# Optimization experiments

Measured on AMD Instinct MI355X. Metric: run time of the kernel, lower is better.

The kernel has to match this reference:

```python
import jax, jax.numpy as jnp
import numpy as np


def setup_inputs() -> dict:
    key = jax.random.key(0)
    ks = jax.random.split(key, 6)
    B, R, H, E, D = 64, 2048, 1024, 512, 1024
    hidden_states = jax.random.normal(ks[0], (B, H), dtype=jnp.float32)
    att_feats = jax.random.normal(ks[1], (B, R, D), dtype=jnp.float32)
    p_att_feats = jax.random.normal(ks[2], (B, R, E), dtype=jnp.float32)
    att_masks = jnp.zeros((B, R), dtype=jnp.float32)  # additive mask; zeros = unmasked
    w_h = jax.random.normal(ks[3], (H, E), dtype=jnp.float32) * (1.0 / np.sqrt(H))
    w_alpha = jax.random.normal(ks[4], (E,), dtype=jnp.float32) * (1.0 / np.sqrt(E))
    return {"hidden_states": hidden_states, "att_feats": att_feats,
            "p_att_feats": p_att_feats, "att_masks": att_masks,
            "w_h": w_h, "w_alpha": w_alpha}


def reference(hidden_states, att_feats, p_att_feats, att_masks, w_h, w_alpha):
    # w_h(hidden_states): [B, E], broadcast over regions R
    wh = hidden_states @ w_h                      # [B, E]
    alpha = jnp.tanh(wh[:, None, :] + p_att_feats)  # [B, R, E]
    # w_alpha reduces E -> scalar per region
    alpha = jnp.einsum('bre,e->br', alpha, w_alpha)  # [B, R]
    alpha = alpha + att_masks                     # additive mask
    alpha = jax.nn.softmax(alpha, axis=-1)        # [B, R]
    # weighted sum over regions: bmm(alpha[:,None,:], att_feats).squeeze(1)
    att = jnp.einsum('br,brd->bd', alpha, att_feats)  # [B, D]
    return att
```

## Files before the change

kernel.cpp:

```cpp
#include <hip/hip_runtime.h>
#include <math.h>

#define BB 64
#define RR 2048
#define HH 1024
#define EE 512
#define DD 1024
#define RC 32
#define RPB (RR / RC)
#define RPW (RPB / 4)

typedef float f32x4 __attribute__((ext_vector_type(4)));

__device__ __forceinline__ float fast_tanh(float x) {
    float e = __expf(2.0f * x);
    return 1.0f - 2.0f * __builtin_amdgcn_rcpf(e + 1.0f);
}

__global__ __launch_bounds__(256) void k_wh(const float* __restrict__ hidden,
                                            const float* __restrict__ w_h,
                                            float* __restrict__ wh) {
    __shared__ float sh[HH];
    __shared__ float sred[4][64];
    const int b = blockIdx.x;
    const int t = threadIdx.x;
    const int lane = t & 63, hseg = t >> 6;
    const int e = blockIdx.y * 64 + lane;
    for (int h = t; h < HH; h += 256) sh[h] = hidden[b * HH + h];
    __syncthreads();
    const int h0 = hseg * 256;
    float acc = 0.f;
#pragma unroll 8
    for (int h = 0; h < 256; ++h) acc = fmaf(sh[h0 + h], w_h[(h0 + h) * EE + e], acc);
    sred[hseg][lane] = acc;
    __syncthreads();
    if (t < 64)
        wh[b * EE + blockIdx.y * 64 + t] =
            (sred[0][t] + sred[1][t]) + (sred[2][t] + sred[3][t]);
}

__global__ __launch_bounds__(256) void k_fused(const float* __restrict__ p_att,
                                               const float* __restrict__ feats,
                                               const float* __restrict__ wh,
                                               const float* __restrict__ w_alpha,
                                               const float* __restrict__ mask,
                                               float* __restrict__ num,
                                               float* __restrict__ den) {
    __shared__ float sw[RPB];
    const int b = blockIdx.x, rc = blockIdx.y;
    const int t = threadIdx.x, wave = t >> 6, lane = t & 63;
    const int r0 = rc * RPB;

    const float* __restrict__ whb = wh + b * EE;
    const f32x4 wh0 = *(const f32x4*)(whb + lane * 4);
    const f32x4 wh1 = *(const f32x4*)(whb + 256 + lane * 4);
    const f32x4 wa0 = *(const f32x4*)(w_alpha + lane * 4);
    const f32x4 wa1 = *(const f32x4*)(w_alpha + 256 + lane * 4);
    const long long rowb = (long long)b * RR + r0 + wave * RPW;
    const f32x4* __restrict__ pb = (const f32x4*)(p_att + rowb * EE);
#pragma unroll 4
    for (int rr = 0; rr < RPW; ++rr) {
        f32x4 p0 = __builtin_nontemporal_load(pb + rr * (EE / 4) + lane);
        f32x4 p1 = __builtin_nontemporal_load(pb + rr * (EE / 4) + 64 + lane);
        float s;
        s = fast_tanh(p0.x + wh0.x) * wa0.x;
        s = fmaf(fast_tanh(p0.y + wh0.y), wa0.y, s);
        s = fmaf(fast_tanh(p0.z + wh0.z), wa0.z, s);
        s = fmaf(fast_tanh(p0.w + wh0.w), wa0.w, s);
        s = fmaf(fast_tanh(p1.x + wh1.x), wa1.x, s);
        s = fmaf(fast_tanh(p1.y + wh1.y), wa1.y, s);
        s = fmaf(fast_tanh(p1.z + wh1.z), wa1.z, s);
        s = fmaf(fast_tanh(p1.w + wh1.w), wa1.w, s);
#pragma unroll
        for (int off = 32; off; off >>= 1) s += __shfl_xor(s, off);
        if (lane == 0) sw[wave * RPW + rr] = __expf(s + mask[rowb + rr]);
    }
    __syncthreads();

    const f32x4* __restrict__ fb =
        (const f32x4*)(feats + ((long long)b * RR + r0) * DD) + t;
    f32x4 acc = {0.f, 0.f, 0.f, 0.f};
#pragma unroll 8
    for (int r = 0; r < RPB; ++r) {
        const float a = sw[r];
        f32x4 f = __builtin_nontemporal_load(fb + r * (DD / 4));
        acc.x = fmaf(a, f.x, acc.x);
        acc.y = fmaf(a, f.y, acc.y);
        acc.z = fmaf(a, f.z, acc.z);
        acc.w = fmaf(a, f.w, acc.w);
    }
    ((f32x4*)(num + (long long)(b * RC + rc) * DD))[t] = acc;
    if (t == 0) {
        float d = 0.f;
#pragma unroll
        for (int r = 0; r < RPB; ++r) d += sw[r];
        den[b * RC + rc] = d;
    }
}

__global__ __launch_bounds__(256) void k_out(const float* __restrict__ num,
                                             const float* __restrict__ den,
                                             float* __restrict__ out) {
    const int idx = blockIdx.x * 256 + threadIdx.x;
    const int b = idx >> 10;
    const int d = idx & 1023;
    float ds = 0.f;
#pragma unroll
    for (int rc = 0; rc < RC; ++rc) ds += den[b * RC + rc];
    float ns = 0.f;
#pragma unroll
    for (int rc = 0; rc < RC; ++rc)
        ns += num[((long long)(b * RC + rc) << 10) + d];
    out[idx] = ns / ds;
}

extern "C" void kernel_launch(void* const* d_in, const int* in_sizes, int n_in,
                              void* d_out, int out_size, void* d_ws, size_t ws_size,
                              hipStream_t stream) {
    const float* hidden  = (const float*)d_in[0];
    const float* feats   = (const float*)d_in[1];
    const float* p_att   = (const float*)d_in[2];
    const float* mask    = (const float*)d_in[3];
    const float* w_h     = (const float*)d_in[4];
    const float* w_alpha = (const float*)d_in[5];
    float* out = (float*)d_out;

    char* ws = (char*)d_ws;
    float* wh  = (float*)(ws);
    float* num = (float*)(ws + (size_t)131072);
    float* den = (float*)(ws + (size_t)(131072 + 8388608));

    k_wh<<<dim3(BB, EE / 64), 256, 0, stream>>>(hidden, w_h, wh);
    k_fused<<<dim3(BB, RC), 256, 0, stream>>>(p_att, feats, wh, w_alpha, mask, num, den);
    k_out<<<(BB * DD) / 256, 256, 0, stream>>>(num, den, out);
}
```

Before: 162.1 us.

## Interleave score and feature accumulation per wave, batch k_wh over multiple rows

The fused kernel no longer computes all softmax weights first and then sweeps features after a barrier. Each wave now weights its own rows' feature vectors as soon as each score is ready, keeping full-width partial sums in registers and reducing the four waves through shared memory at the end. This is meant to overlap the p_att and feature streams and remove the mid-kernel barrier stall, at the cost of more registers and a 16KB shared reduction buffer. Other changes: nontemporal loads are dropped, the grid axes are swapped, and k_wh processes four batch rows per block to reuse w_h loads.

```diff
diff --git a/kernel.cpp b/kernel.cpp
--- a/kernel.cpp
+++ b/kernel.cpp
@@ -9,6 +9,7 @@
 #define RC 32
 #define RPB (RR / RC)
 #define RPW (RPB / 4)
+#define MB 4
 
 typedef float f32x4 __attribute__((ext_vector_type(4)));
 
@@ -17,26 +18,42 @@
     return 1.0f - 2.0f * __builtin_amdgcn_rcpf(e + 1.0f);
 }
 
+__device__ __forceinline__ f32x4 fma4(float a, f32x4 f, f32x4 c) {
+    c.x = fmaf(a, f.x, c.x);
+    c.y = fmaf(a, f.y, c.y);
+    c.z = fmaf(a, f.z, c.z);
+    c.w = fmaf(a, f.w, c.w);
+    return c;
+}
+
 __global__ __launch_bounds__(256) void k_wh(const float* __restrict__ hidden,
                                             const float* __restrict__ w_h,
                                             float* __restrict__ wh) {
-    __shared__ float sh[HH];
-    __shared__ float sred[4][64];
-    const int b = blockIdx.x;
+    __shared__ float sh[MB][HH];
+    __shared__ float sred[4][MB][64];
+    const int b0 = blockIdx.x * MB;
     const int t = threadIdx.x;
     const int lane = t & 63, hseg = t >> 6;
     const int e = blockIdx.y * 64 + lane;
-    for (int h = t; h < HH; h += 256) sh[h] = hidden[b * HH + h];
+    for (int idx = t; idx < MB * HH; idx += 256)
+        ((float*)sh)[idx] = hidden[b0 * HH + idx];
     __syncthreads();
     const int h0 = hseg * 256;
-    float acc = 0.f;
-#pragma unroll 8
-    for (int h = 0; h < 256; ++h) acc = fmaf(sh[h0 + h], w_h[(h0 + h) * EE + e], acc);
-    sred[hseg][lane] = acc;
+    float acc[MB] = {0.f, 0.f, 0.f, 0.f};
+#pragma unroll 4
+    for (int h = 0; h < 256; ++h) {
+        const float wv = w_h[(h0 + h) * EE + e];
+#pragma unroll
+        for (int b = 0; b < MB; ++b) acc[b] = fmaf(sh[b][h0 + h], wv, acc[b]);
+    }
+#pragma unroll
+    for (int b = 0; b < MB; ++b) sred[hseg][b][lane] = acc[b];
     __syncthreads();
-    if (t < 64)
-        wh[b * EE + blockIdx.y * 64 + t] =
-            (sred[0][t] + sred[1][t]) + (sred[2][t] + sred[3][t]);
+    if (t < MB * 64) {
+        const int b = t >> 6, l = t & 63;
+        wh[(b0 + b) * EE + blockIdx.y * 64 + l] =
+            (sred[0][b][l] + sred[1][b][l]) + (sred[2][b][l] + sred[3][b][l]);
+    }
 }
 
 __global__ __launch_bounds__(256) void k_fused(const float* __restrict__ p_att,
@@ -46,22 +63,27 @@
                                                const float* __restrict__ mask,
                                                float* __restrict__ num,
                                                float* __restrict__ den) {
-    __shared__ float sw[RPB];
-    const int b = blockIdx.x, rc = blockIdx.y;
+    __shared__ float snum[4][DD];
+    __shared__ float sden[4];
+    const int rc = blockIdx.x, b = blockIdx.y;
     const int t = threadIdx.x, wave = t >> 6, lane = t & 63;
-    const int r0 = rc * RPB;
 
     const float* __restrict__ whb = wh + b * EE;
     const f32x4 wh0 = *(const f32x4*)(whb + lane * 4);
     const f32x4 wh1 = *(const f32x4*)(whb + 256 + lane * 4);
     const f32x4 wa0 = *(const f32x4*)(w_alpha + lane * 4);
     const f32x4 wa1 = *(const f32x4*)(w_alpha + 256 + lane * 4);
-    const long long rowb = (long long)b * RR + r0 + wave * RPW;
-    const f32x4* __restrict__ pb = (const f32x4*)(p_att + rowb * EE);
-#pragma unroll 4
+
+    const long long row0 = (long long)b * RR + rc * RPB + wave * RPW;
+    const f32x4* __restrict__ pb = (const f32x4*)(p_att + row0 * EE);
+    const f32x4* __restrict__ fb = (const f32x4*)(feats + row0 * DD);
+
+    f32x4 acc0 = {0.f, 0.f, 0.f, 0.f}, acc1 = acc0, acc2 = acc0, acc3 = acc0;
+    float dsum = 0.f;
+#pragma unroll 2
     for (int rr = 0; rr < RPW; ++rr) {
-        f32x4 p0 = __builtin_nontemporal_load(pb + rr * (EE / 4) + lane);
-        f32x4 p1 = __builtin_nontemporal_load(pb + rr * (EE / 4) + 64 + lane);
+        f32x4 p0 = pb[rr * (EE / 4) + lane];
+        f32x4 p1 = pb[rr * (EE / 4) + 64 + lane];
         float s;
         s = fast_tanh(p0.x + wh0.x) * wa0.x;
         s = fmaf(fast_tanh(p0.y + wh0.y), wa0.y, s);
@@ -73,29 +95,27 @@
         s = fmaf(fast_tanh(p1.w + wh1.w), wa1.w, s);
 #pragma unroll
         for (int off = 32; off; off >>= 1) s += __shfl_xor(s, off);
-        if (lane == 0) sw[wave * RPW + rr] = __expf(s + mask[rowb + rr]);
+        const float w = __expf(s + mask[row0 + rr]);
+        dsum += w;
+        const f32x4* __restrict__ fr = fb + rr * (DD / 4);
+        acc0 = fma4(w, fr[lane], acc0);
+        acc1 = fma4(w, fr[64 + lane], acc1);
+        acc2 = fma4(w, fr[128 + lane], acc2);
+        acc3 = fma4(w, fr[192 + lane], acc3);
     }
+    *(f32x4*)&snum[wave][0 + lane * 4] = acc0;
+    *(f32x4*)&snum[wave][256 + lane * 4] = acc1;
+    *(f32x4*)&snum[wave][512 + lane * 4] = acc2;
+    *(f32x4*)&snum[wave][768 + lane * 4] = acc3;
+    if (lane == 0) sden[wave] = dsum;
     __syncthreads();
-
-    const f32x4* __restrict__ fb =
-        (const f32x4*)(feats + ((long long)b * RR + r0) * DD) + t;
-    f32x4 acc = {0.f, 0.f, 0.f, 0.f};
-#pragma unroll 8
-    for (int r = 0; r < RPB; ++r) {
-        const float a = sw[r];
-        f32x4 f = __builtin_nontemporal_load(fb + r * (DD / 4));
-        acc.x = fmaf(a, f.x, acc.x);
-        acc.y = fmaf(a, f.y, acc.y);
-        acc.z = fmaf(a, f.z, acc.z);
-        acc.w = fmaf(a, f.w, acc.w);
-    }
-    ((f32x4*)(num + (long long)(b * RC + rc) * DD))[t] = acc;
-    if (t == 0) {
-        float d = 0.f;
-#pragma unroll
-        for (int r = 0; r < RPB; ++r) d += sw[r];
-        den[b * RC + rc] = d;
-    }
+    f32x4 r0 = *(const f32x4*)&snum[0][t * 4];
+    f32x4 r1 = *(const f32x4*)&snum[1][t * 4];
+    f32x4 r2 = *(const f32x4*)&snum[2][t * 4];
+    f32x4 r3 = *(const f32x4*)&snum[3][t * 4];
+    f32x4 r = (r0 + r1) + (r2 + r3);
+    ((f32x4*)(num + (long long)(b * RC + rc) * DD))[t] = r;
+    if (t == 0) den[b * RC + rc] = (sden[0] + sden[1]) + (sden[2] + sden[3]);
 }
 
 __global__ __launch_bounds__(256) void k_out(const float* __restrict__ num,
@@ -130,7 +150,7 @@
     float* num = (float*)(ws + (size_t)131072);
     float* den = (float*)(ws + (size_t)(131072 + 8388608));
 
-    k_wh<<<dim3(BB, EE / 64), 256, 0, stream>>>(hidden, w_h, wh);
-    k_fused<<<dim3(BB, RC), 256, 0, stream>>>(p_att, feats, wh, w_alpha, mask, num, den);
+    k_wh<<<dim3(BB / MB, EE / 64), 256, 0, stream>>>(hidden, w_h, wh);
+    k_fused<<<dim3(RC, BB), 256, 0, stream>>>(p_att, feats, wh, w_alpha, mask, num, den);
     k_out<<<(BB * DD) / 256, 256, 0, stream>>>(num, den, out);
 }
```

New measurement: 199.3 us. 22.9% more time.

## Batch four rows per k_wh block and halve region chunks in fused kernel

Applied to the files above, without the earlier changes.

k_wh now handles four batch rows per block, so each w_h element loaded from global memory feeds four accumulators. This cuts w_h traffic fourfold and launches fewer blocks. Separately, RC drops from 32 to 16, so each k_fused block covers twice as many regions. That halves the partial-sum buffer and the k_out reduction work, but leaves 1024 fused blocks with longer serial loops, which may hide memory latency less well.

```diff
diff --git a/kernel.cpp b/kernel.cpp
--- a/kernel.cpp
+++ b/kernel.cpp
@@ -6,9 +6,10 @@
 #define HH 1024
 #define EE 512
 #define DD 1024
-#define RC 32
+#define RC 16
 #define RPB (RR / RC)
 #define RPW (RPB / 4)
+#define MB 4
 
 typedef float f32x4 __attribute__((ext_vector_type(4)));
 
@@ -20,23 +21,31 @@
 __global__ __launch_bounds__(256) void k_wh(const float* __restrict__ hidden,
                                             const float* __restrict__ w_h,
                                             float* __restrict__ wh) {
-    __shared__ float sh[HH];
-    __shared__ float sred[4][64];
-    const int b = blockIdx.x;
+    __shared__ float sh[MB][HH];
+    __shared__ float sred[4][MB][64];
+    const int b0 = blockIdx.x * MB;
     const int t = threadIdx.x;
     const int lane = t & 63, hseg = t >> 6;
     const int e = blockIdx.y * 64 + lane;
-    for (int h = t; h < HH; h += 256) sh[h] = hidden[b * HH + h];
+    for (int idx = t; idx < MB * HH; idx += 256)
+        ((float*)sh)[idx] = hidden[b0 * HH + idx];
     __syncthreads();
     const int h0 = hseg * 256;
-    float acc = 0.f;
-#pragma unroll 8
-    for (int h = 0; h < 256; ++h) acc = fmaf(sh[h0 + h], w_h[(h0 + h) * EE + e], acc);
-    sred[hseg][lane] = acc;
+    float acc[MB] = {0.f, 0.f, 0.f, 0.f};
+#pragma unroll 4
+    for (int h = 0; h < 256; ++h) {
+        const float wv = w_h[(h0 + h) * EE + e];
+#pragma unroll
+        for (int b = 0; b < MB; ++b) acc[b] = fmaf(sh[b][h0 + h], wv, acc[b]);
+    }
+#pragma unroll
+    for (int b = 0; b < MB; ++b) sred[hseg][b][lane] = acc[b];
     __syncthreads();
-    if (t < 64)
-        wh[b * EE + blockIdx.y * 64 + t] =
-            (sred[0][t] + sred[1][t]) + (sred[2][t] + sred[3][t]);
+    if (t < MB * 64) {
+        const int b = t >> 6, l = t & 63;
+        wh[(b0 + b) * EE + blockIdx.y * 64 + l] =
+            (sred[0][b][l] + sred[1][b][l]) + (sred[2][b][l] + sred[3][b][l]);
+    }
 }
 
 __global__ __launch_bounds__(256) void k_fused(const float* __restrict__ p_att,
@@ -128,9 +137,9 @@
     char* ws = (char*)d_ws;
     float* wh  = (float*)(ws);
     float* num = (float*)(ws + (size_t)131072);
-    float* den = (float*)(ws + (size_t)(131072 + 8388608));
+    float* den = (float*)(ws + (size_t)(131072 + 4194304));
 
-    k_wh<<<dim3(BB, EE / 64), 256, 0, stream>>>(hidden, w_h, wh);
+    k_wh<<<dim3(BB / MB, EE / 64), 256, 0, stream>>>(hidden, w_h, wh);
     k_fused<<<dim3(BB, RC), 256, 0, stream>>>(p_att, feats, wh, w_alpha, mask, num, den);
     k_out<<<(BB * DD) / 256, 256, 0, stream>>>(num, den, out);
 }
```

New measurement: 164.3 us. Within noise of the previous version (+1.3%).
